# Optimization experiments

Hardware: AMD Instinct MI355X
Metric: run time of the kernel (lower is better)

Reference implementation:

```python
import jax, jax.numpy as jnp
import numpy as np

IOU_THRESHOLDS = (0.5, 0.75)
B, N, G = 256, 4000, 50


def _iou(amin, amax, bmin, bmax):
    # broadcasted temporal IoU: anchors [N,1] vs boxes [1,G] -> [N,G]
    inter = jnp.maximum(jnp.minimum(amax, bmax) - jnp.maximum(amin, bmin), 0.0)
    union = (amax - amin) + (bmax - bmin) - inter
    return inter / union


def _greedy_tp(segments, gts, thr):
    # segments: [N,2], gts: [G,2]. Replicates AP.get_values greedy matching:
    # for each label (in order), claim the first (lowest-index) unused proposal
    # whose IoU > thr. Final used-mask == is_TP.
    ious = _iou(segments[:, 0:1], segments[:, 1:2], gts[None, :, 0], gts[None, :, 1])  # [N,G]
    pot = ious > thr
    n = segments.shape[0]

    def step(used, col):  # col: [N] bool, candidates for this label
        cand = col & ~used
        idx = jnp.argmax(cand)  # first True (argmax of bool is first max)
        used = jnp.where(jnp.any(cand), used.at[idx].set(True), used)
        return used, None

    used, _ = jax.lax.scan(step, jnp.zeros((n,), jnp.bool_), pot.T)
    return used  # [N] bool


def _ap_for_threshold(scores, segments, labels, thr):
    is_tp = jax.vmap(lambda s, g: _greedy_tp(s, g, thr))(segments, labels)  # [B,N]
    conf = scores.reshape(-1)                       # [B*N]
    tp = is_tp.reshape(-1).astype(jnp.float32)
    order = jnp.argsort(-conf)                      # sort by confidence, descending
    tp = tp[order]
    n_labels = labels.shape[0] * labels.shape[1]
    m = tp.shape[0]
    acc_tp = jnp.cumsum(tp)
    precision = acc_tp / (jnp.arange(m, dtype=jnp.float32) + 1.0)
    recall = acc_tp / jnp.float32(n_labels)
    # curve = [[1,0]] then (recall, precision) reversed; AP = sum(|dx| * cummax(y)[:-1])
    x = jnp.concatenate([jnp.ones((1,), jnp.float32), recall[::-1]])
    y = jnp.concatenate([jnp.zeros((1,), jnp.float32), precision[::-1]])
    y_max = jax.lax.cummax(y, axis=0)
    x_diff = jnp.abs(jnp.diff(x))
    return jnp.sum(x_diff * y_max[:-1])


def setup_inputs() -> dict:
    key = jax.random.key(0)
    k1, k2, k3, k4, k5 = jax.random.split(key, 5)
    scores = jax.random.uniform(k1, (B, N), dtype=jnp.float32)
    p_start = jax.random.uniform(k2, (B, N), dtype=jnp.float32) * 0.9
    p_len = jax.random.uniform(k3, (B, N), dtype=jnp.float32) * 0.1 + 0.005
    segments = jnp.stack([p_start, p_start + p_len], axis=-1)  # [B,N,2], start<end
    g_start = jax.random.uniform(k4, (B, G), dtype=jnp.float32) * 0.9
    g_len = jax.random.uniform(k5, (B, G), dtype=jnp.float32) * 0.1 + 0.005
    labels = jnp.stack([g_start, g_start + g_len], axis=-1)    # [B,G,2]
    return {"scores": scores, "segments": segments, "labels": labels}


def reference(scores, segments, labels):
    # returns AP at each IoU threshold, shape [len(IOU_THRESHOLDS)]
    return jnp.stack([_ap_for_threshold(scores, segments, labels, t) for t in IOU_THRESHOLDS])
```

## Files before the change

kernel.cpp:

```cpp
#include <hip/hip_runtime.h>


#define B_ 256
#define N_ 4000
#define G_ 50
#define M_ (B_ * N_)
#define NL_ (B_ * G_)
#define NBKT 2048

#define M0_ 0x1.000001p-1
#define M1_ 0x1.800001p-1

typedef unsigned long long u64;

__device__ __forceinline__ unsigned bucket_of(float c) {
    unsigned b = (unsigned)(c * 2048.0f);
    return b > (NBKT - 1) ? (NBKT - 1) : b;
}

__global__ __launch_bounds__(1024) void tp_kernel(
    const float* __restrict__ seg,
    const float* __restrict__ gts,
    const float* __restrict__ conf,
    int* __restrict__ tpIdx,
    int* __restrict__ cnt,
    unsigned short* __restrict__ pbh)
{
    const int tid  = threadIdx.x;
    const int lane = tid & 63;
    const int wv   = tid >> 6;
    const int b    = blockIdx.x;

    __shared__ float2 gtl[G_];
    __shared__ u64 cand[2][G_][64];
    __shared__ unsigned hls[NBKT];
    __shared__ int lcnt[2];

    #pragma unroll
    for (int k = 0; k < NBKT / 1024; ++k) hls[k * 1024 + tid] = 0u;
    if (tid < G_) gtl[tid] = ((const float2*)gts)[b * G_ + tid];
    if (tid < 2) lcnt[tid] = 0;
    __syncthreads();

    const float* cb = conf + (size_t)b * N_;
    #pragma unroll
    for (int s = 0; s < 4; ++s) {
        int n = s * 1024 + tid;
        if (n < N_) atomicAdd(&hls[bucket_of(cb[n])], 1u);
    }

    const float2* sb = (const float2*)(seg + (size_t)b * (N_ * 2));
    float pmin[4], pmax[4], plen[4];
    #pragma unroll
    for (int s = 0; s < 4; ++s) {
        int n = s * 1024 + tid;
        if (n < N_) { float2 v = sb[n]; pmin[s] = v.x; pmax[s] = v.y; }
        else { pmin[s] = 1e9f; pmax[s] = 1e9f; }
        plen[s] = pmax[s] - pmin[s];
    }
    for (int g = 0; g < G_; ++g) {
        float2 gt = gtl[g];
        float glen = gt.y - gt.x;
        u64 m0[4], m1[4];
        #pragma unroll
        for (int s = 0; s < 4; ++s) {
            float inter = fmaxf(fminf(pmax[s], gt.y) - fmaxf(pmin[s], gt.x), 0.0f);
            float uni = plen[s] + glen - inter;
            double di = (double)inter;
            double du = (double)uni;
            m0[s] = __ballot(di > M0_ * du);
            m1[s] = __ballot(di > M1_ * du);
        }
        if (lane == 0) {
            #pragma unroll
            for (int s = 0; s < 4; ++s) {
                cand[0][g][s * 16 + wv] = m0[s];
                cand[1][g][s * 16 + wv] = m1[s];
            }
        }
    }
    __syncthreads();

    #pragma unroll
    for (int k = 0; k < NBKT / 1024; ++k) {
        int bin = k * 1024 + tid;
        pbh[(size_t)b * NBKT + bin] = (unsigned short)hls[bin];
    }

    if (wv < 2) {
        const int thr_i = wv;
        u64 used = 0ull;
        for (int g = 0; g < G_; ++g) {
            u64 c = cand[thr_i][g][lane] & ~used;
            u64 ball = __ballot(c != 0ull);
            if (ball) {
                int fl = __ffsll(ball) - 1;
                if (lane == fl) used |= (c & (0ull - c));
            }
        }
        int cpop = __popcll(used);
        if (cpop) {
            int j = atomicAdd(&lcnt[thr_i], cpop);
            u64 u = used;
            while (u) {
                int bit = __ffsll(u) - 1;
                u &= u - 1;
                tpIdx[thr_i * NL_ + b * G_ + j++] = b * N_ + lane * 64 + bit;
            }
        }
    }
    __syncthreads();
    if (tid < 2) cnt[tid * B_ + b] = lcnt[tid];
}

__global__ __launch_bounds__(256) void s1_kernel(
    unsigned short* __restrict__ pbh,
    unsigned* __restrict__ total)
{
    __shared__ unsigned sc[256];
    const int bin = blockIdx.x;
    const int b = threadIdx.x;
    unsigned v = pbh[(size_t)b * NBKT + bin];
    sc[b] = v;
    __syncthreads();
    for (int off = 1; off < 256; off <<= 1) {
        unsigned add = (b >= off) ? sc[b - off] : 0u;
        __syncthreads();
        sc[b] += add;
        __syncthreads();
    }
    pbh[(size_t)b * NBKT + bin] = (unsigned short)(sc[b] - v);
    if (b == 255) total[bin] = sc[255];
}

__global__ __launch_bounds__(1024) void s2_kernel(
    const unsigned* __restrict__ total, unsigned* __restrict__ binStart)
{
    __shared__ unsigned part[1024];
    int t = threadIdx.x;
    uint2 v2 = ((const uint2*)total)[t];
    unsigned s = v2.x + v2.y;
    part[t] = s;
    __syncthreads();
    for (int off = 1; off < 1024; off <<= 1) {
        unsigned add = (t >= off) ? part[t - off] : 0u;
        __syncthreads();
        part[t] += add;
        __syncthreads();
    }
    unsigned base = (t == 0) ? 0u : part[t - 1];
    ((uint2*)binStart)[t] = make_uint2(base, base + v2.x);
}

__global__ __launch_bounds__(1024) void scatter_kernel(
    const float* __restrict__ conf,
    const unsigned short* __restrict__ pbh,
    const unsigned* __restrict__ binStart,
    u64* __restrict__ sKey)
{
    __shared__ unsigned baseB[NBKT];
    __shared__ unsigned lofs[NBKT];
    const int tid = threadIdx.x;
    const int b = blockIdx.x;
    #pragma unroll
    for (int k = 0; k < NBKT / 1024; ++k) {
        int bin = k * 1024 + tid;
        baseB[bin] = binStart[bin] + pbh[(size_t)b * NBKT + bin];
        lofs[bin] = 0u;
    }
    __syncthreads();
    const float* cb = conf + (size_t)b * N_;
    #pragma unroll
    for (int s = 0; s < 4; ++s) {
        int n = s * 1024 + tid;
        if (n < N_) {
            float c = cb[n];
            unsigned bin = bucket_of(c);
            unsigned lo = atomicAdd(&lofs[bin], 1u);
            unsigned idx = (unsigned)(b * N_ + n);
            sKey[baseB[bin] + lo] = ((u64)__float_as_uint(c) << 32) | (u64)(0xFFFFFFFFu - idx);
        }
    }
}

__global__ __launch_bounds__(256) void rank_kernel(
    const float* __restrict__ conf,
    const int* __restrict__ tpIdx,
    const int* __restrict__ cnt,
    const unsigned* __restrict__ total,
    const unsigned* __restrict__ binStart,
    const u64* __restrict__ sKey,
    int* __restrict__ tpRank)
{
    const int lane = threadIdx.x & 63;
    const int w = (blockIdx.x << 2) | (threadIdx.x >> 6);
    if (w >= 2 * NL_) return;
    const int thr_i = w / NL_;
    const int t = w - thr_i * NL_;
    const int batch = t / G_;
    const int j = t - batch * G_;

    if (j < cnt[thr_i * B_ + batch]) {
        int e = tpIdx[thr_i * NL_ + t];
        float c = conf[e];
        u64 keyE = ((u64)__float_as_uint(c) << 32) | (u64)(0xFFFFFFFFu - (unsigned)e);
        unsigned bin = bucket_of(c);
        unsigned lo = binStart[bin], n = total[bin];
        int r = M_ - (int)lo - (int)n;
        for (unsigned base = 0; base < n; base += 64) {
            unsigned k = base + lane;
            bool pred = (k < n) && (sKey[lo + k] > keyE);
            r += (int)__popcll(__ballot(pred));
        }
        if (lane == 0) tpRank[thr_i * NL_ + t] = r;
    } else {
        if (lane == 0) tpRank[thr_i * NL_ + t] = M_ + t;
    }
}

__global__ __launch_bounds__(1024) void sortap_kernel(
    const int* __restrict__ tpRank,
    float* __restrict__ out)
{
    const int C = 13;
    union U1 { unsigned part[1024]; float cmax[1024]; };
    union U2 { unsigned hist[NBKT]; double red[1024]; };
    __shared__ int sr[NL_];
    __shared__ U1 u1;
    __shared__ U2 u2;
    const int thr_i = blockIdx.x;
    const int t = threadIdx.x;

    u2.hist[t] = 0u; u2.hist[t + 1024] = 0u;
    __syncthreads();

    int r[C]; unsigned beta[C];
    #pragma unroll
    for (int k = 0; k < C; ++k) {
        int i = t + k * 1024;
        if (i < NL_) {
            int rr = tpRank[thr_i * NL_ + i];
            r[k] = rr;
            unsigned bb = ((unsigned)rr) >> 9;
            beta[k] = bb > (NBKT - 1) ? (NBKT - 1) : bb;
            atomicAdd(&u2.hist[beta[k]], 1u);
        } else { r[k] = 0; beta[k] = 0xFFFFFFFFu; }
    }
    __syncthreads();

    unsigned h0 = u2.hist[2 * t], h1 = u2.hist[2 * t + 1];
    u1.part[t] = h0 + h1;
    __syncthreads();
    for (int off = 1; off < 1024; off <<= 1) {
        unsigned add = (t >= off) ? u1.part[t - off] : 0u;
        __syncthreads();
        u1.part[t] += add;
        __syncthreads();
    }
    unsigned base = (t == 0) ? 0u : u1.part[t - 1];
    __syncthreads();
    u2.hist[2 * t] = base;
    u2.hist[2 * t + 1] = base + h0;
    __syncthreads();

    #pragma unroll
    for (int k = 0; k < C; ++k)
        if (beta[k] != 0xFFFFFFFFu) {
            unsigned slot = atomicAdd(&u2.hist[beta[k]], 1u);
            sr[slot] = r[k];
        }
    __syncthreads();

    int p[C];
    #pragma unroll
    for (int k = 0; k < C; ++k) {
        if (beta[k] != 0xFFFFFFFFu) {
            unsigned st = (beta[k] == 0u) ? 0u : u2.hist[beta[k] - 1];
            unsigned en = u2.hist[beta[k]];
            int c = 0;
            for (unsigned j = st; j < en; ++j) c += (sr[j] < r[k]);
            p[k] = (int)st + c;
        } else p[k] = -1;
    }
    __syncthreads();
    #pragma unroll
    for (int k = 0; k < C; ++k)
        if (p[k] >= 0) sr[p[k]] = r[k];
    __syncthreads();

    float pr[C]; int rk[C];
    #pragma unroll
    for (int k = 0; k < C; ++k) {
        int i = t * C + k;
        rk[k] = (i < NL_) ? sr[i] : 0x7FFFFFFF;
        pr[k] = (rk[k] < M_) ? (float)(i + 1) / (float)(rk[k] + 1) : -1.0f;
    }
    float suf[C];
    float run = -1.0f;
    #pragma unroll
    for (int k = C - 1; k >= 0; --k) { run = fmaxf(run, pr[k]); suf[k] = run; }

    u1.cmax[t] = run;
    __syncthreads();
    for (int off = 1; off < 1024; off <<= 1) {
        float v = u1.cmax[t];
        float o = (t + off < 1024) ? u1.cmax[t + off] : -1.0f;
        __syncthreads();
        u1.cmax[t] = fmaxf(v, o);
        __syncthreads();
    }
    float follow = (t + 1 < 1024) ? u1.cmax[t + 1] : -1.0f;

    double acc = 0.0;
    #pragma unroll
    for (int k = 0; k < C; ++k) {
        int i = t * C + k;
        if (rk[k] >= 1 && rk[k] < M_) {
            float smax = fmaxf(suf[k], follow);
            float rhi = (float)(i + 1) / 12800.0f;
            float rlo = (float)i / 12800.0f;
            acc += (double)((rhi - rlo) * smax);
        }
    }
    __syncthreads();
    u2.red[t] = acc;
    __syncthreads();
    for (int off = 512; off >= 1; off >>= 1) {
        if (t < off) u2.red[t] += u2.red[t + off];
        __syncthreads();
    }
    if (t == 0) out[thr_i] = (float)u2.red[0];
}

extern "C" void kernel_launch(void* const* d_in, const int* in_sizes, int n_in,
                              void* d_out, int out_size, void* d_ws, size_t ws_size,
                              hipStream_t stream) {
    const float* scores = (const float*)d_in[0];
    const float* seg    = (const float*)d_in[1];
    const float* gts    = (const float*)d_in[2];
    float* out = (float*)d_out;

    char* p = (char*)d_ws;
    int*            cnt        = (int*)p;             p += 4096;
    int*            tpIdx      = (int*)p;             p += 2 * NL_ * 4;
    int*            tpRank     = (int*)p;             p += 2 * NL_ * 4;
    unsigned*       total      = (unsigned*)p;        p += NBKT * 4;
    unsigned*       binStart   = (unsigned*)p;        p += NBKT * 4;
    unsigned short* pbh        = (unsigned short*)p;  p += (size_t)B_ * NBKT * 2;
    u64*            sKey       = (u64*)p;             p += (size_t)M_ * 8;
    (void)ws_size; (void)in_sizes; (void)n_in; (void)out_size;

    tp_kernel<<<B_, 1024, 0, stream>>>(seg, gts, scores, tpIdx, cnt, pbh);
    s1_kernel<<<NBKT, 256, 0, stream>>>(pbh, total);
    s2_kernel<<<1, 1024, 0, stream>>>(total, binStart);
    scatter_kernel<<<B_, 1024, 0, stream>>>(scores, pbh, binStart, sKey);
    rank_kernel<<<(2 * NL_ + 3) / 4, 256, 0, stream>>>(scores, tpIdx, cnt,
                                                       total, binStart, sKey, tpRank);
    sortap_kernel<<<2, 1024, 0, stream>>>(tpRank, out);
}
```

Before: 169.8 us.

## Fuse six pipeline kernels into one cooperative kernel with grid syncs

Merges the TP matching, per-bin scan, global bin scan, scatter, rank and AP kernels into a single cooperative launch of 256 blocks, using grid.sync between phases and a shared-memory union. Each block now also recomputes the global bin-offset scan redundantly instead of a separate single-block kernel. The aim is to remove five kernel launch gaps. In exchange, the rank phase runs on only 256 blocks instead of many, and the final AP phase leaves 254 blocks idle at the end.

```diff
diff --git a/kernel.cpp b/kernel.cpp
--- a/kernel.cpp
+++ b/kernel.cpp
@@ -1,4 +1,7 @@
 #include <hip/hip_runtime.h>
+#include <hip/hip_cooperative_groups.h>
+
+namespace cg = cooperative_groups;
 
 
 #define B_ 256
@@ -18,318 +21,316 @@
     return b > (NBKT - 1) ? (NBKT - 1) : b;
 }
 
-__global__ __launch_bounds__(1024) void tp_kernel(
+struct TpS {
+    float2 gtl[G_];
+    u64 cand[2][G_][64];
+    unsigned hls[NBKT];
+    int lcnt[2];
+};
+struct S1S { unsigned sc[4][256]; };
+struct ScS { unsigned baseB[NBKT]; unsigned lofs[NBKT]; };
+struct ApS {
+    int sr[NL_];
+    union { unsigned part[1024]; float cmax[1024]; } u1;
+    union { unsigned hist[NBKT]; double red[1024]; } u2;
+};
+union SmemU { TpS tp; S1S s1; ScS sc; ApS ap; };
+
+__global__ __launch_bounds__(1024) void mega_kernel(
     const float* __restrict__ seg,
     const float* __restrict__ gts,
     const float* __restrict__ conf,
     int* __restrict__ tpIdx,
     int* __restrict__ cnt,
-    unsigned short* __restrict__ pbh)
+    unsigned short* __restrict__ pbh,
+    unsigned* __restrict__ total,
+    unsigned* __restrict__ binStartG,
+    u64* __restrict__ sKey,
+    int* __restrict__ tpRank,
+    float* __restrict__ out)
 {
+    cg::grid_group grid = cg::this_grid();
     const int tid  = threadIdx.x;
     const int lane = tid & 63;
     const int wv   = tid >> 6;
     const int b    = blockIdx.x;
 
-    __shared__ float2 gtl[G_];
-    __shared__ u64 cand[2][G_][64];
-    __shared__ unsigned hls[NBKT];
-    __shared__ int lcnt[2];
-
-    #pragma unroll
-    for (int k = 0; k < NBKT / 1024; ++k) hls[k * 1024 + tid] = 0u;
-    if (tid < G_) gtl[tid] = ((const float2*)gts)[b * G_ + tid];
-    if (tid < 2) lcnt[tid] = 0;
-    __syncthreads();
-
-    const float* cb = conf + (size_t)b * N_;
-    #pragma unroll
-    for (int s = 0; s < 4; ++s) {
-        int n = s * 1024 + tid;
-        if (n < N_) atomicAdd(&hls[bucket_of(cb[n])], 1u);
-    }
-
-    const float2* sb = (const float2*)(seg + (size_t)b * (N_ * 2));
-    float pmin[4], pmax[4], plen[4];
-    #pragma unroll
-    for (int s = 0; s < 4; ++s) {
-        int n = s * 1024 + tid;
-        if (n < N_) { float2 v = sb[n]; pmin[s] = v.x; pmax[s] = v.y; }
-        else { pmin[s] = 1e9f; pmax[s] = 1e9f; }
-        plen[s] = pmax[s] - pmin[s];
-    }
-    for (int g = 0; g < G_; ++g) {
-        float2 gt = gtl[g];
-        float glen = gt.y - gt.x;
-        u64 m0[4], m1[4];
+    __shared__ SmemU smem;
+
+    {
+        #pragma unroll
+        for (int k = 0; k < NBKT / 1024; ++k) smem.tp.hls[k * 1024 + tid] = 0u;
+        if (tid < G_) smem.tp.gtl[tid] = ((const float2*)gts)[b * G_ + tid];
+        if (tid < 2) smem.tp.lcnt[tid] = 0;
+        __syncthreads();
+
+        const float* cb = conf + (size_t)b * N_;
         #pragma unroll
         for (int s = 0; s < 4; ++s) {
-            float inter = fmaxf(fminf(pmax[s], gt.y) - fmaxf(pmin[s], gt.x), 0.0f);
-            float uni = plen[s] + glen - inter;
-            double di = (double)inter;
-            double du = (double)uni;
-            m0[s] = __ballot(di > M0_ * du);
-            m1[s] = __ballot(di > M1_ * du);
-        }
-        if (lane == 0) {
+            int n = s * 1024 + tid;
+            if (n < N_) atomicAdd(&smem.tp.hls[bucket_of(cb[n])], 1u);
+        }
+
+        const float2* sb = (const float2*)(seg + (size_t)b * (N_ * 2));
+        float pmin[4], pmax[4], plen[4];
+        #pragma unroll
+        for (int s = 0; s < 4; ++s) {
+            int n = s * 1024 + tid;
+            if (n < N_) { float2 v = sb[n]; pmin[s] = v.x; pmax[s] = v.y; }
+            else { pmin[s] = 1e9f; pmax[s] = 1e9f; }
+            plen[s] = pmax[s] - pmin[s];
+        }
+        for (int g = 0; g < G_; ++g) {
+            float2 gt = smem.tp.gtl[g];
+            float glen = gt.y - gt.x;
+            u64 m0[4], m1[4];
             #pragma unroll
             for (int s = 0; s < 4; ++s) {
-                cand[0][g][s * 16 + wv] = m0[s];
-                cand[1][g][s * 16 + wv] = m1[s];
-            }
-        }
-    }
-    __syncthreads();
-
-    #pragma unroll
-    for (int k = 0; k < NBKT / 1024; ++k) {
-        int bin = k * 1024 + tid;
-        pbh[(size_t)b * NBKT + bin] = (unsigned short)hls[bin];
-    }
-
-    if (wv < 2) {
-        const int thr_i = wv;
-        u64 used = 0ull;
-        for (int g = 0; g < G_; ++g) {
-            u64 c = cand[thr_i][g][lane] & ~used;
-            u64 ball = __ballot(c != 0ull);
-            if (ball) {
-                int fl = __ffsll(ball) - 1;
-                if (lane == fl) used |= (c & (0ull - c));
-            }
-        }
-        int cpop = __popcll(used);
-        if (cpop) {
-            int j = atomicAdd(&lcnt[thr_i], cpop);
-            u64 u = used;
-            while (u) {
-                int bit = __ffsll(u) - 1;
-                u &= u - 1;
-                tpIdx[thr_i * NL_ + b * G_ + j++] = b * N_ + lane * 64 + bit;
-            }
-        }
-    }
-    __syncthreads();
-    if (tid < 2) cnt[tid * B_ + b] = lcnt[tid];
-}
-
-__global__ __launch_bounds__(256) void s1_kernel(
-    unsigned short* __restrict__ pbh,
-    unsigned* __restrict__ total)
-{
-    __shared__ unsigned sc[256];
-    const int bin = blockIdx.x;
-    const int b = threadIdx.x;
-    unsigned v = pbh[(size_t)b * NBKT + bin];
-    sc[b] = v;
-    __syncthreads();
-    for (int off = 1; off < 256; off <<= 1) {
-        unsigned add = (b >= off) ? sc[b - off] : 0u;
-        __syncthreads();
-        sc[b] += add;
-        __syncthreads();
-    }
-    pbh[(size_t)b * NBKT + bin] = (unsigned short)(sc[b] - v);
-    if (b == 255) total[bin] = sc[255];
-}
-
-__global__ __launch_bounds__(1024) void s2_kernel(
-    const unsigned* __restrict__ total, unsigned* __restrict__ binStart)
-{
-    __shared__ unsigned part[1024];
-    int t = threadIdx.x;
-    uint2 v2 = ((const uint2*)total)[t];
-    unsigned s = v2.x + v2.y;
-    part[t] = s;
-    __syncthreads();
-    for (int off = 1; off < 1024; off <<= 1) {
-        unsigned add = (t >= off) ? part[t - off] : 0u;
-        __syncthreads();
-        part[t] += add;
-        __syncthreads();
-    }
-    unsigned base = (t == 0) ? 0u : part[t - 1];
-    ((uint2*)binStart)[t] = make_uint2(base, base + v2.x);
-}
-
-__global__ __launch_bounds__(1024) void scatter_kernel(
-    const float* __restrict__ conf,
-    const unsigned short* __restrict__ pbh,
-    const unsigned* __restrict__ binStart,
-    u64* __restrict__ sKey)
-{
-    __shared__ unsigned baseB[NBKT];
-    __shared__ unsigned lofs[NBKT];
-    const int tid = threadIdx.x;
-    const int b = blockIdx.x;
-    #pragma unroll
-    for (int k = 0; k < NBKT / 1024; ++k) {
-        int bin = k * 1024 + tid;
-        baseB[bin] = binStart[bin] + pbh[(size_t)b * NBKT + bin];
-        lofs[bin] = 0u;
-    }
-    __syncthreads();
-    const float* cb = conf + (size_t)b * N_;
-    #pragma unroll
-    for (int s = 0; s < 4; ++s) {
-        int n = s * 1024 + tid;
-        if (n < N_) {
-            float c = cb[n];
-            unsigned bin = bucket_of(c);
-            unsigned lo = atomicAdd(&lofs[bin], 1u);
-            unsigned idx = (unsigned)(b * N_ + n);
-            sKey[baseB[bin] + lo] = ((u64)__float_as_uint(c) << 32) | (u64)(0xFFFFFFFFu - idx);
-        }
-    }
-}
-
-__global__ __launch_bounds__(256) void rank_kernel(
-    const float* __restrict__ conf,
-    const int* __restrict__ tpIdx,
-    const int* __restrict__ cnt,
-    const unsigned* __restrict__ total,
-    const unsigned* __restrict__ binStart,
-    const u64* __restrict__ sKey,
-    int* __restrict__ tpRank)
-{
-    const int lane = threadIdx.x & 63;
-    const int w = (blockIdx.x << 2) | (threadIdx.x >> 6);
-    if (w >= 2 * NL_) return;
-    const int thr_i = w / NL_;
-    const int t = w - thr_i * NL_;
-    const int batch = t / G_;
-    const int j = t - batch * G_;
-
-    if (j < cnt[thr_i * B_ + batch]) {
-        int e = tpIdx[thr_i * NL_ + t];
-        float c = conf[e];
-        u64 keyE = ((u64)__float_as_uint(c) << 32) | (u64)(0xFFFFFFFFu - (unsigned)e);
-        unsigned bin = bucket_of(c);
-        unsigned lo = binStart[bin], n = total[bin];
-        int r = M_ - (int)lo - (int)n;
-        for (unsigned base = 0; base < n; base += 64) {
-            unsigned k = base + lane;
-            bool pred = (k < n) && (sKey[lo + k] > keyE);
-            r += (int)__popcll(__ballot(pred));
-        }
-        if (lane == 0) tpRank[thr_i * NL_ + t] = r;
-    } else {
-        if (lane == 0) tpRank[thr_i * NL_ + t] = M_ + t;
-    }
-}
-
-__global__ __launch_bounds__(1024) void sortap_kernel(
-    const int* __restrict__ tpRank,
-    float* __restrict__ out)
-{
-    const int C = 13;
-    union U1 { unsigned part[1024]; float cmax[1024]; };
-    union U2 { unsigned hist[NBKT]; double red[1024]; };
-    __shared__ int sr[NL_];
-    __shared__ U1 u1;
-    __shared__ U2 u2;
-    const int thr_i = blockIdx.x;
-    const int t = threadIdx.x;
-
-    u2.hist[t] = 0u; u2.hist[t + 1024] = 0u;
-    __syncthreads();
-
-    int r[C]; unsigned beta[C];
-    #pragma unroll
-    for (int k = 0; k < C; ++k) {
-        int i = t + k * 1024;
-        if (i < NL_) {
-            int rr = tpRank[thr_i * NL_ + i];
-            r[k] = rr;
-            unsigned bb = ((unsigned)rr) >> 9;
-            beta[k] = bb > (NBKT - 1) ? (NBKT - 1) : bb;
-            atomicAdd(&u2.hist[beta[k]], 1u);
-        } else { r[k] = 0; beta[k] = 0xFFFFFFFFu; }
-    }
-    __syncthreads();
-
-    unsigned h0 = u2.hist[2 * t], h1 = u2.hist[2 * t + 1];
-    u1.part[t] = h0 + h1;
-    __syncthreads();
-    for (int off = 1; off < 1024; off <<= 1) {
-        unsigned add = (t >= off) ? u1.part[t - off] : 0u;
-        __syncthreads();
-        u1.part[t] += add;
-        __syncthreads();
-    }
-    unsigned base = (t == 0) ? 0u : u1.part[t - 1];
-    __syncthreads();
-    u2.hist[2 * t] = base;
-    u2.hist[2 * t + 1] = base + h0;
-    __syncthreads();
-
-    #pragma unroll
-    for (int k = 0; k < C; ++k)
-        if (beta[k] != 0xFFFFFFFFu) {
-            unsigned slot = atomicAdd(&u2.hist[beta[k]], 1u);
-            sr[slot] = r[k];
-        }
-    __syncthreads();
-
-    int p[C];
-    #pragma unroll
-    for (int k = 0; k < C; ++k) {
-        if (beta[k] != 0xFFFFFFFFu) {
-            unsigned st = (beta[k] == 0u) ? 0u : u2.hist[beta[k] - 1];
-            unsigned en = u2.hist[beta[k]];
-            int c = 0;
-            for (unsigned j = st; j < en; ++j) c += (sr[j] < r[k]);
-            p[k] = (int)st + c;
-        } else p[k] = -1;
-    }
-    __syncthreads();
-    #pragma unroll
-    for (int k = 0; k < C; ++k)
-        if (p[k] >= 0) sr[p[k]] = r[k];
-    __syncthreads();
-
-    float pr[C]; int rk[C];
-    #pragma unroll
-    for (int k = 0; k < C; ++k) {
-        int i = t * C + k;
-        rk[k] = (i < NL_) ? sr[i] : 0x7FFFFFFF;
-        pr[k] = (rk[k] < M_) ? (float)(i + 1) / (float)(rk[k] + 1) : -1.0f;
-    }
-    float suf[C];
-    float run = -1.0f;
-    #pragma unroll
-    for (int k = C - 1; k >= 0; --k) { run = fmaxf(run, pr[k]); suf[k] = run; }
-
-    u1.cmax[t] = run;
-    __syncthreads();
-    for (int off = 1; off < 1024; off <<= 1) {
-        float v = u1.cmax[t];
-        float o = (t + off < 1024) ? u1.cmax[t + off] : -1.0f;
-        __syncthreads();
-        u1.cmax[t] = fmaxf(v, o);
-        __syncthreads();
-    }
-    float follow = (t + 1 < 1024) ? u1.cmax[t + 1] : -1.0f;
-
-    double acc = 0.0;
-    #pragma unroll
-    for (int k = 0; k < C; ++k) {
-        int i = t * C + k;
-        if (rk[k] >= 1 && rk[k] < M_) {
-            float smax = fmaxf(suf[k], follow);
-            float rhi = (float)(i + 1) / 12800.0f;
-            float rlo = (float)i / 12800.0f;
-            acc += (double)((rhi - rlo) * smax);
-        }
-    }
-    __syncthreads();
-    u2.red[t] = acc;
-    __syncthreads();
-    for (int off = 512; off >= 1; off >>= 1) {
-        if (t < off) u2.red[t] += u2.red[t + off];
-        __syncthreads();
-    }
-    if (t == 0) out[thr_i] = (float)u2.red[0];
+                float inter = fmaxf(fminf(pmax[s], gt.y) - fmaxf(pmin[s], gt.x), 0.0f);
+                float uni = plen[s] + glen - inter;
+                double di = (double)inter;
+                double du = (double)uni;
+                m0[s] = __ballot(di > M0_ * du);
+                m1[s] = __ballot(di > M1_ * du);
+            }
+            if (lane == 0) {
+                #pragma unroll
+                for (int s = 0; s < 4; ++s) {
+                    smem.tp.cand[0][g][s * 16 + wv] = m0[s];
+                    smem.tp.cand[1][g][s * 16 + wv] = m1[s];
+                }
+            }
+        }
+        __syncthreads();
+
+        #pragma unroll
+        for (int k = 0; k < NBKT / 1024; ++k) {
+            int bin = k * 1024 + tid;
+            pbh[(size_t)b * NBKT + bin] = (unsigned short)smem.tp.hls[bin];
+        }
+
+        if (wv < 2) {
+            const int thr_i = wv;
+            u64 used = 0ull;
+            for (int g = 0; g < G_; ++g) {
+                u64 c = smem.tp.cand[thr_i][g][lane] & ~used;
+                u64 ball = __ballot(c != 0ull);
+                if (ball) {
+                    int fl = __ffsll(ball) - 1;
+                    if (lane == fl) used |= (c & (0ull - c));
+                }
+            }
+            int cpop = __popcll(used);
+            if (cpop) {
+                int j = atomicAdd(&smem.tp.lcnt[thr_i], cpop);
+                u64 u = used;
+                while (u) {
+                    int bit = __ffsll(u) - 1;
+                    u &= u - 1;
+                    tpIdx[thr_i * NL_ + b * G_ + j++] = b * N_ + lane * 64 + bit;
+                }
+            }
+        }
+        __syncthreads();
+        if (tid < 2) cnt[tid * B_ + b] = smem.tp.lcnt[tid];
+    }
+    grid.sync();
+
+    {
+        unsigned* sc = smem.s1.sc[tid >> 8];
+        const int bb = tid & 255;
+        #pragma unroll
+        for (int r2 = 0; r2 < 2; ++r2) {
+            const int bin = b * 8 + r2 * 4 + (tid >> 8);
+            unsigned v = pbh[(size_t)bb * NBKT + bin];
+            sc[bb] = v;
+            __syncthreads();
+            for (int off = 1; off < 256; off <<= 1) {
+                unsigned add = (bb >= off) ? sc[bb - off] : 0u;
+                __syncthreads();
+                sc[bb] += add;
+                __syncthreads();
+            }
+            pbh[(size_t)bb * NBKT + bin] = (unsigned short)(sc[bb] - v);
+            if (bb == 255) total[bin] = sc[255];
+            __syncthreads();
+        }
+    }
+    grid.sync();
+
+    {
+        unsigned* part = smem.sc.lofs;
+        uint2 v2 = ((const uint2*)total)[tid];
+        unsigned s = v2.x + v2.y;
+        part[tid] = s;
+        __syncthreads();
+        for (int off = 1; off < 1024; off <<= 1) {
+            unsigned add = (tid >= off) ? part[tid - off] : 0u;
+            __syncthreads();
+            part[tid] += add;
+            __syncthreads();
+        }
+        unsigned base = (tid == 0) ? 0u : part[tid - 1];
+        __syncthreads();
+        smem.sc.baseB[2 * tid]     = base;
+        smem.sc.baseB[2 * tid + 1] = base + v2.x;
+        __syncthreads();
+        #pragma unroll
+        for (int k = 0; k < 2; ++k) {
+            int bin = k * 1024 + tid;
+            unsigned bs = smem.sc.baseB[bin];
+            if (b == 0) binStartG[bin] = bs;
+            smem.sc.baseB[bin] = bs + pbh[(size_t)b * NBKT + bin];
+            smem.sc.lofs[bin] = 0u;
+        }
+        __syncthreads();
+        const float* cb = conf + (size_t)b * N_;
+        #pragma unroll
+        for (int s4 = 0; s4 < 4; ++s4) {
+            int n = s4 * 1024 + tid;
+            if (n < N_) {
+                float c = cb[n];
+                unsigned bin = bucket_of(c);
+                unsigned lo = atomicAdd(&smem.sc.lofs[bin], 1u);
+                unsigned idx = (unsigned)(b * N_ + n);
+                sKey[smem.sc.baseB[bin] + lo] =
+                    ((u64)__float_as_uint(c) << 32) | (u64)(0xFFFFFFFFu - idx);
+            }
+        }
+    }
+    grid.sync();
+
+    {
+        for (int w = (b << 4) | wv; w < 2 * NL_; w += B_ * 16) {
+            const int thr_i = w / NL_;
+            const int t = w - thr_i * NL_;
+            const int batch = t / G_;
+            const int j = t - batch * G_;
+            if (j < cnt[thr_i * B_ + batch]) {
+                int e = tpIdx[thr_i * NL_ + t];
+                float c = conf[e];
+                u64 keyE = ((u64)__float_as_uint(c) << 32) |
+                           (u64)(0xFFFFFFFFu - (unsigned)e);
+                unsigned bin = bucket_of(c);
+                unsigned lo = binStartG[bin], n = total[bin];
+                int r = M_ - (int)lo - (int)n;
+                for (unsigned base2 = 0; base2 < n; base2 += 64) {
+                    unsigned k = base2 + lane;
+                    bool pred = (k < n) && (sKey[lo + k] > keyE);
+                    r += (int)__popcll(__ballot(pred));
+                }
+                if (lane == 0) tpRank[thr_i * NL_ + t] = r;
+            } else {
+                if (lane == 0) tpRank[thr_i * NL_ + t] = M_ + t;
+            }
+        }
+    }
+    grid.sync();
+
+    if (b < 2) {
+        const int C = 13;
+        const int thr_i = b;
+
+        smem.ap.u2.hist[tid] = 0u; smem.ap.u2.hist[tid + 1024] = 0u;
+        __syncthreads();
+
+        int r[C]; unsigned beta[C];
+        #pragma unroll
+        for (int k = 0; k < C; ++k) {
+            int i = tid + k * 1024;
+            if (i < NL_) {
+                int rr = tpRank[thr_i * NL_ + i];
+                r[k] = rr;
+                unsigned bb = ((unsigned)rr) >> 9;
+                beta[k] = bb > (NBKT - 1) ? (NBKT - 1) : bb;
+                atomicAdd(&smem.ap.u2.hist[beta[k]], 1u);
+            } else { r[k] = 0; beta[k] = 0xFFFFFFFFu; }
+        }
+        __syncthreads();
+
+        unsigned h0 = smem.ap.u2.hist[2 * tid], h1 = smem.ap.u2.hist[2 * tid + 1];
+        smem.ap.u1.part[tid] = h0 + h1;
+        __syncthreads();
+        for (int off = 1; off < 1024; off <<= 1) {
+            unsigned add = (tid >= off) ? smem.ap.u1.part[tid - off] : 0u;
+            __syncthreads();
+            smem.ap.u1.part[tid] += add;
+            __syncthreads();
+        }
+        unsigned base = (tid == 0) ? 0u : smem.ap.u1.part[tid - 1];
+        __syncthreads();
+        smem.ap.u2.hist[2 * tid] = base;
+        smem.ap.u2.hist[2 * tid + 1] = base + h0;
+        __syncthreads();
+
+        #pragma unroll
+        for (int k = 0; k < C; ++k)
+            if (beta[k] != 0xFFFFFFFFu) {
+                unsigned slot = atomicAdd(&smem.ap.u2.hist[beta[k]], 1u);
+                smem.ap.sr[slot] = r[k];
+            }
+        __syncthreads();
+
+        int p[C];
+        #pragma unroll
+        for (int k = 0; k < C; ++k) {
+            if (beta[k] != 0xFFFFFFFFu) {
+                unsigned st = (beta[k] == 0u) ? 0u : smem.ap.u2.hist[beta[k] - 1];
+                unsigned en = smem.ap.u2.hist[beta[k]];
+                int c = 0;
+                for (unsigned j = st; j < en; ++j) c += (smem.ap.sr[j] < r[k]);
+                p[k] = (int)st + c;
+            } else p[k] = -1;
+        }
+        __syncthreads();
+        #pragma unroll
+        for (int k = 0; k < C; ++k)
+            if (p[k] >= 0) smem.ap.sr[p[k]] = r[k];
+        __syncthreads();
+
+        float pr[C]; int rk[C];
+        #pragma unroll
+        for (int k = 0; k < C; ++k) {
+            int i = tid * C + k;
+            rk[k] = (i < NL_) ? smem.ap.sr[i] : 0x7FFFFFFF;
+            pr[k] = (rk[k] < M_) ? (float)(i + 1) / (float)(rk[k] + 1) : -1.0f;
+        }
+        float suf[C];
+        float run = -1.0f;
+        #pragma unroll
+        for (int k = C - 1; k >= 0; --k) { run = fmaxf(run, pr[k]); suf[k] = run; }
+
+        smem.ap.u1.cmax[tid] = run;
+        __syncthreads();
+        for (int off = 1; off < 1024; off <<= 1) {
+            float v = smem.ap.u1.cmax[tid];
+            float o = (tid + off < 1024) ? smem.ap.u1.cmax[tid + off] : -1.0f;
+            __syncthreads();
+            smem.ap.u1.cmax[tid] = fmaxf(v, o);
+            __syncthreads();
+        }
+        float follow = (tid + 1 < 1024) ? smem.ap.u1.cmax[tid + 1] : -1.0f;
+
+        double acc = 0.0;
+        #pragma unroll
+        for (int k = 0; k < C; ++k) {
+            int i = tid * C + k;
+            if (rk[k] >= 1 && rk[k] < M_) {
+                float smax = fmaxf(suf[k], follow);
+                float rhi = (float)(i + 1) / 12800.0f;
+                float rlo = (float)i / 12800.0f;
+                acc += (double)((rhi - rlo) * smax);
+            }
+        }
+        __syncthreads();
+        smem.ap.u2.red[tid] = acc;
+        __syncthreads();
+        for (int off = 512; off >= 1; off >>= 1) {
+            if (tid < off) smem.ap.u2.red[tid] += smem.ap.u2.red[tid + off];
+            __syncthreads();
+        }
+        if (tid == 0) out[thr_i] = (float)smem.ap.u2.red[0];
+    }
 }
 
 extern "C" void kernel_launch(void* const* d_in, const int* in_sizes, int n_in,
@@ -350,11 +351,10 @@
     u64*            sKey       = (u64*)p;             p += (size_t)M_ * 8;
     (void)ws_size; (void)in_sizes; (void)n_in; (void)out_size;
 
-    tp_kernel<<<B_, 1024, 0, stream>>>(seg, gts, scores, tpIdx, cnt, pbh);
-    s1_kernel<<<NBKT, 256, 0, stream>>>(pbh, total);
-    s2_kernel<<<1, 1024, 0, stream>>>(total, binStart);
-    scatter_kernel<<<B_, 1024, 0, stream>>>(scores, pbh, binStart, sKey);
-    rank_kernel<<<(2 * NL_ + 3) / 4, 256, 0, stream>>>(scores, tpIdx, cnt,
-                                                       total, binStart, sKey, tpRank);
-    sortap_kernel<<<2, 1024, 0, stream>>>(tpRank, out);
+    void* args[] = { (void*)&seg, (void*)&gts, (void*)&scores,
+                     (void*)&tpIdx, (void*)&cnt, (void*)&pbh,
+                     (void*)&total, (void*)&binStart, (void*)&sKey,
+                     (void*)&tpRank, (void*)&out };
+    hipLaunchCooperativeKernel(mega_kernel, dim3(B_), dim3(1024),
+                               args, 0, stream);
 }
```

Result: slower. 308.3 us (+81.5%).

## Fuse bin-total scan into scatter kernel and tile per-batch histogram scan

Applied to the files above, without the earlier changes.

The per-bin column scan over batches now runs as 64 blocks that load a 256x32 tile of the histogram into shared memory with 16-byte loads and scan each column serially, instead of 2048 blocks each doing a strided Hillis-Steele scan. The global exclusive scan over bin totals is folded into every scatter block, which removes one kernel launch; block 0 writes binStart for the later rank kernel. This cuts launch count and uncoalesced accesses, but every scatter block now repeats the 1024-wide scan redundantly.

```diff
diff --git a/kernel.cpp b/kernel.cpp
--- a/kernel.cpp
+++ b/kernel.cpp
@@ -117,62 +117,71 @@
     unsigned short* __restrict__ pbh,
     unsigned* __restrict__ total)
 {
-    __shared__ unsigned sc[256];
-    const int bin = blockIdx.x;
-    const int b = threadIdx.x;
-    unsigned v = pbh[(size_t)b * NBKT + bin];
-    sc[b] = v;
-    __syncthreads();
-    for (int off = 1; off < 256; off <<= 1) {
-        unsigned add = (b >= off) ? sc[b - off] : 0u;
-        __syncthreads();
-        sc[b] += add;
-        __syncthreads();
-    }
-    pbh[(size_t)b * NBKT + bin] = (unsigned short)(sc[b] - v);
-    if (b == 255) total[bin] = sc[255];
-}
-
-__global__ __launch_bounds__(1024) void s2_kernel(
-    const unsigned* __restrict__ total, unsigned* __restrict__ binStart)
-{
-    __shared__ unsigned part[1024];
-    int t = threadIdx.x;
-    uint2 v2 = ((const uint2*)total)[t];
-    unsigned s = v2.x + v2.y;
-    part[t] = s;
-    __syncthreads();
-    for (int off = 1; off < 1024; off <<= 1) {
-        unsigned add = (t >= off) ? part[t - off] : 0u;
-        __syncthreads();
-        part[t] += add;
-        __syncthreads();
-    }
-    unsigned base = (t == 0) ? 0u : part[t - 1];
-    ((uint2*)binStart)[t] = make_uint2(base, base + v2.x);
+    __shared__ unsigned short tile[256][32];
+    const int j = blockIdx.x;
+    const int t = threadIdx.x;
+    uint4* dst = (uint4*)&tile[t][0];
+    const uint4* src = (const uint4*)(pbh + (size_t)t * NBKT + j * 32);
+    #pragma unroll
+    for (int k = 0; k < 4; ++k) dst[k] = src[k];
+    __syncthreads();
+    if (t < 32) {
+        unsigned run = 0;
+        for (int b = 0; b < 256; ++b) {
+            unsigned v = tile[b][t];
+            tile[b][t] = (unsigned short)run;
+            run += v;
+        }
+        total[j * 32 + t] = run;
+    }
+    __syncthreads();
+    uint4* back = (uint4*)(pbh + (size_t)t * NBKT + j * 32);
+    #pragma unroll
+    for (int k = 0; k < 4; ++k) back[k] = dst[k];
 }
 
 __global__ __launch_bounds__(1024) void scatter_kernel(
     const float* __restrict__ conf,
     const unsigned short* __restrict__ pbh,
-    const unsigned* __restrict__ binStart,
+    const unsigned* __restrict__ total,
+    unsigned* __restrict__ binStartG,
     u64* __restrict__ sKey)
 {
     __shared__ unsigned baseB[NBKT];
     __shared__ unsigned lofs[NBKT];
     const int tid = threadIdx.x;
     const int b = blockIdx.x;
-    #pragma unroll
-    for (int k = 0; k < NBKT / 1024; ++k) {
+
+    unsigned* part = lofs;
+    uint2 v2 = ((const uint2*)total)[tid];
+    unsigned s = v2.x + v2.y;
+    part[tid] = s;
+    __syncthreads();
+    for (int off = 1; off < 1024; off <<= 1) {
+        unsigned add = (tid >= off) ? part[tid - off] : 0u;
+        __syncthreads();
+        part[tid] += add;
+        __syncthreads();
+    }
+    unsigned base = (tid == 0) ? 0u : part[tid - 1];
+    __syncthreads();
+    baseB[2 * tid]     = base;
+    baseB[2 * tid + 1] = base + v2.x;
+    __syncthreads();
+    #pragma unroll
+    for (int k = 0; k < 2; ++k) {
         int bin = k * 1024 + tid;
-        baseB[bin] = binStart[bin] + pbh[(size_t)b * NBKT + bin];
+        unsigned bs = baseB[bin];
+        if (b == 0) binStartG[bin] = bs;
+        baseB[bin] = bs + pbh[(size_t)b * NBKT + bin];
         lofs[bin] = 0u;
     }
     __syncthreads();
+
     const float* cb = conf + (size_t)b * N_;
     #pragma unroll
-    for (int s = 0; s < 4; ++s) {
-        int n = s * 1024 + tid;
+    for (int s4 = 0; s4 < 4; ++s4) {
+        int n = s4 * 1024 + tid;
         if (n < N_) {
             float c = cb[n];
             unsigned bin = bucket_of(c);
@@ -351,9 +360,8 @@
     (void)ws_size; (void)in_sizes; (void)n_in; (void)out_size;
 
     tp_kernel<<<B_, 1024, 0, stream>>>(seg, gts, scores, tpIdx, cnt, pbh);
-    s1_kernel<<<NBKT, 256, 0, stream>>>(pbh, total);
-    s2_kernel<<<1, 1024, 0, stream>>>(total, binStart);
-    scatter_kernel<<<B_, 1024, 0, stream>>>(scores, pbh, binStart, sKey);
+    s1_kernel<<<64, 256, 0, stream>>>(pbh, total);
+    scatter_kernel<<<B_, 1024, 0, stream>>>(scores, pbh, total, binStart, sKey);
     rank_kernel<<<(2 * NL_ + 3) / 4, 256, 0, stream>>>(scores, tpIdx, cnt,
                                                        total, binStart, sKey, tpRank);
     sortap_kernel<<<2, 1024, 0, stream>>>(tpRank, out);
```

New measurement: 168.1 us. No clear change (-1.0%).
